# Kernel tuning notes

Hardware: AMD Instinct MI355X
Metric: run time of the kernel (lower is better)

The kernel has to match this reference:

```python
import jax, jax.numpy as jnp
import numpy as np


def setup_inputs() -> dict:
    key = jax.random.key(0)
    k1, k2, k3, k4 = jax.random.split(key, 4)
    B, T, E, H = 8, 2048, 1024, 64
    x = jax.random.normal(k1, (B, T, E), dtype=jnp.float32)
    # scale params like typical init to keep logits sane
    Wk = jax.random.normal(k2, (E, H), dtype=jnp.float32) * (E ** -0.5)
    Wq = jax.random.normal(k3, (E, H), dtype=jnp.float32) * (E ** -0.5)
    Wv = jax.random.normal(k4, (E, H), dtype=jnp.float32) * (E ** -0.5)
    return {"x": x, "Wk": Wk, "Wq": Wq, "Wv": Wv}


def reference(x, Wk, Wq, Wv):
    # x: [B, T, E]; Wk/Wq/Wv: [E, H]
    T = x.shape[1]
    H = Wk.shape[1]
    k = jnp.einsum('bte,eh->bth', x, Wk)
    q = jnp.einsum('bte,eh->bth', x, Wq)
    v = jnp.einsum('bte,eh->bth', x, Wv)
    # scaled scores [B, T, T]
    wei = jnp.einsum('bqh,bkh->bqk', q, k) * (H ** -0.5)
    causal = jnp.tril(jnp.ones((T, T), dtype=bool))  # tril buffer
    wei = jnp.where(causal, wei, -jnp.inf)
    wei = jax.nn.softmax(wei, axis=-1)
    # dropout p=0.0 (eval): identity
    return jnp.einsum('bqk,bkh->bqh', wei, v)
```

## Files before the change

kernel.cpp:

```cpp
#include <hip/hip_runtime.h>
#include <math.h>

constexpr int B_ = 8, T_ = 2048, E_ = 1024, H_ = 64;
constexpr long BT = (long)B_ * T_;

typedef __attribute__((ext_vector_type(8))) short bf16x8;
typedef __attribute__((ext_vector_type(4))) float f32x4;

__device__ inline unsigned short bf16_rne(float f) {
    union { float f; unsigned u; } v; v.f = f;
    unsigned u = v.u + (0x7FFFu + ((v.u >> 16) & 1u));
    return (unsigned short)(u >> 16);
}
__device__ inline unsigned pack_bf16x2(float lo, float hi) {
    return (unsigned)bf16_rne(lo) | ((unsigned)bf16_rne(hi) << 16);
}

__device__ inline void load_lds16(const void* g, void* l) {
    __builtin_amdgcn_global_load_lds(
        (const __attribute__((address_space(1))) void*)(uintptr_t)g,
        (__attribute__((address_space(3))) void*)(unsigned)(uintptr_t)l,
        16, 0, 0);
}

constexpr float QS = 0.18033688011112042f;

__global__ __launch_bounds__(256) void wt_build_k(
    const float* __restrict__ Wk, const float* __restrict__ Wq,
    const float* __restrict__ Wv, unsigned short* __restrict__ Wt)
{
    const int d    = blockIdx.x * 256 + threadIdx.x;
    const int tile = d >> 6;
    const int lq   = d & 63;
    const int quad = lq >> 4;
    const int l16  = lq & 15;
    const int kc   = tile / 12;
    const int nt   = tile - kc * 12;
    const int n    = nt * 16 + l16;

    const float* src; int col; float s = 1.0f;
    if (n < 64)       { src = Wk; col = n; }
    else if (n < 128) { src = Wq; col = n - 64; s = QS; }
    else              { src = Wv; col = n - 128; }

    const int kk0 = kc * 32 + quad * 8;
    const float* sp = src + (size_t)kk0 * H_ + col;
    unsigned p[4];
    #pragma unroll
    for (int jj = 0; jj < 4; jj++)
        p[jj] = pack_bf16x2(sp[(2 * jj) * H_] * s, sp[(2 * jj + 1) * H_] * s);
    *(uint4*)(Wt + (size_t)d * 8) = make_uint4(p[0], p[1], p[2], p[3]);
}

__global__ __launch_bounds__(512, 4) void qkv_mfma_k(
    const float* __restrict__ x, const unsigned short* __restrict__ Wt,
    unsigned short* __restrict__ kO, unsigned short* __restrict__ qO,
    unsigned short* __restrict__ vfO)
{
    __shared__ float4 xs[2][32][16];
    __shared__ unsigned short VL[32][66];

    const int t    = threadIdx.x;
    const int w    = t >> 6;
    const int l    = t & 63;
    const int l16  = l & 15;
    const int quad = l >> 4;
    const int rg   = w >> 2;
    const int nq   = w & 3;
    const int row0 = blockIdx.x * 32 + rg * 16;
    const int row0b = blockIdx.x * 32;

    const int rr = w * 4 + (l >> 4);
    const int cc = l & 15;
    const int gg = cc ^ (rr & 7);
    const float* gsrc = x + (size_t)(row0b + rr) * E_ + gg * 4;

    const int r  = rg * 16 + l16;
    const int rx = r & 7;

    f32x4 acc[3];
    #pragma unroll
    for (int n = 0; n < 3; n++) acc[n] = (f32x4){0.f, 0.f, 0.f, 0.f};

    load_lds16(gsrc, &xs[0][rr][cc]);

    for (int it = 0; it < 16; ++it) {
        const int buf = it & 1;
        __syncthreads();
        if (it + 1 < 16)
            load_lds16(gsrc + (it + 1) * 64, &xs[buf ^ 1][rr][cc]);

        #pragma unroll
        for (int kk = 0; kk < 2; ++kk) {
            const int G0 = kk * 8 + quad * 2;
            float4 fa = xs[buf][r][G0 ^ rx];
            float4 fb = xs[buf][r][(G0 + 1) ^ rx];

            const int kc = it * 2 + kk;
            const unsigned short* wpp = Wt + (size_t)(kc * 12 + nq * 3) * 512 + (size_t)l * 8;
            bf16x8 b0 = *(const bf16x8*)(wpp);
            bf16x8 b1 = *(const bf16x8*)(wpp + 512);
            bf16x8 b2 = *(const bf16x8*)(wpp + 1024);

            union { bf16x8 v; unsigned u[4]; } av;
            av.u[0] = pack_bf16x2(fa.x, fa.y);
            av.u[1] = pack_bf16x2(fa.z, fa.w);
            av.u[2] = pack_bf16x2(fb.x, fb.y);
            av.u[3] = pack_bf16x2(fb.z, fb.w);

            acc[0] = __builtin_amdgcn_mfma_f32_16x16x32_bf16(av.v, b0, acc[0], 0, 0, 0);
            acc[1] = __builtin_amdgcn_mfma_f32_16x16x32_bf16(av.v, b1, acc[1], 0, 0, 0);
            acc[2] = __builtin_amdgcn_mfma_f32_16x16x32_bf16(av.v, b2, acc[2], 0, 0, 0);
        }
    }

    #pragma unroll
    for (int n = 0; n < 3; n++) {
        const int gn = nq * 3 + n;
        const int hb = gn * 16 + l16;
        if (gn < 4) {
            #pragma unroll
            for (int rr2 = 0; rr2 < 4; rr2++) {
                const int row = row0 + quad * 4 + rr2;
                kO[(size_t)row * H_ + hb] = bf16_rne(acc[n][rr2]);
            }
        } else if (gn < 8) {
            #pragma unroll
            for (int rr2 = 0; rr2 < 4; rr2++) {
                const int row = row0 + quad * 4 + rr2;
                qO[(size_t)row * H_ + (hb - 64)] = bf16_rne(acc[n][rr2]);
            }
        } else {
            #pragma unroll
            for (int rr2 = 0; rr2 < 4; rr2++)
                VL[rg * 16 + quad * 4 + rr2][(gn - 8) * 16 + l16] = bf16_rne(acc[n][rr2]);
        }
    }
    __syncthreads();

    if (t < 256) {
        const int g  = t >> 6;
        const int lf = t & 15;
        const int qf = (t >> 4) & 3;
        unsigned pk[4];
        #pragma unroll
        for (int jj = 0; jj < 4; jj++) {
            const int p0 = qf * 8 + 2 * jj;
            const int i0 = (p0 >> 1) | ((p0 & 1) << 4);
            const int p1 = p0 + 1;
            const int i1 = (p1 >> 1) | ((p1 & 1) << 4);
            pk[jj] = (unsigned)VL[i0][g * 16 + lf]
                   | ((unsigned)VL[i1][g * 16 + lf] << 16);
        }
        const int tile = blockIdx.x;
        *(uint4*)(vfO + ((size_t)tile * 4 + g) * 512 + (size_t)(t & 63) * 8) =
            make_uint4(pk[0], pk[1], pk[2], pk[3]);
    }
}

__global__ __launch_bounds__(256, 2) void attn_mfma(
    const unsigned short* __restrict__ q,
    const unsigned short* __restrict__ k,
    const unsigned short* __restrict__ vf,
    float* __restrict__ out)
{
    __shared__ __align__(16) unsigned short KV[4][2][4096];
    __shared__ unsigned short Pl[4][16 * 40];

    const int t    = threadIdx.x;
    const int w    = t >> 6;
    const int l    = t & 63;
    const int l16  = l & 15;
    const int quad = l >> 4;

    const int b    = blockIdx.x & 7;
    const int qidx = blockIdx.x >> 3;
    const int qt   = (qidx & 1) ? (127 - (qidx >> 1)) : (qidx >> 1);
    const int t0   = qt * 16;
    const int nk   = t0 / 32 + 1;

    const size_t qoff = ((size_t)b * T_ + t0 + l16) * H_ + quad * 8;
    bf16x8 aq0 = *(const bf16x8*)(q + qoff);
    bf16x8 aq1 = *(const bf16x8*)(q + qoff + 32);

    f32x4 o[4];
    #pragma unroll
    for (int g = 0; g < 4; g++) o[g] = (f32x4){0.f, 0.f, 0.f, 0.f};
    float ls[4] = {0.f, 0.f, 0.f, 0.f};

    const unsigned short* kbp = k  + (size_t)b * T_ * H_;
    const unsigned short* vfb = vf + (size_t)b * 64 * 2048;
    unsigned short* Pw = &Pl[w][0];
    unsigned short* kv0 = &KV[w][0][0];
    unsigned short* kv1 = &KV[w][1][0];

    auto issue_tile = [&](int kt, unsigned short* dst) {
        const int kbase = kt * 32;
        const unsigned short* kp = kbp + (size_t)(kbase + l16) * H_ + quad * 8;
        load_lds16(kp,               dst + 0 * 512 + l * 8);
        load_lds16(kp + 32,          dst + 1 * 512 + l * 8);
        load_lds16(kp + 16 * H_,     dst + 2 * 512 + l * 8);
        load_lds16(kp + 16 * H_ + 32, dst + 3 * 512 + l * 8);
        const unsigned short* vp = vfb + (size_t)kt * 2048 + l * 8;
        load_lds16(vp,        dst + 4 * 512 + l * 8);
        load_lds16(vp + 512,  dst + 5 * 512 + l * 8);
        load_lds16(vp + 1024, dst + 6 * 512 + l * 8);
        load_lds16(vp + 1536, dst + 7 * 512 + l * 8);
    };

    if (w < nk) issue_tile(w, kv0);

    int it = 0;
    for (int kt = w; kt < nk; kt += 4, ++it) {
        unsigned short* cur = (it & 1) ? kv1 : kv0;
        unsigned short* nxt = (it & 1) ? kv0 : kv1;
        if (kt + 4 < nk) {
            issue_tile(kt + 4, nxt);
            asm volatile("s_waitcnt vmcnt(8)" ::: "memory");
        } else {
            asm volatile("s_waitcnt vmcnt(0)" ::: "memory");
        }

        bf16x8 bk00 = *(const bf16x8*)(cur + 0 * 512 + l * 8);
        bf16x8 bk01 = *(const bf16x8*)(cur + 1 * 512 + l * 8);
        bf16x8 bk10 = *(const bf16x8*)(cur + 2 * 512 + l * 8);
        bf16x8 bk11 = *(const bf16x8*)(cur + 3 * 512 + l * 8);
        bf16x8 bv0  = *(const bf16x8*)(cur + 4 * 512 + l * 8);
        bf16x8 bv1  = *(const bf16x8*)(cur + 5 * 512 + l * 8);
        bf16x8 bv2  = *(const bf16x8*)(cur + 6 * 512 + l * 8);
        bf16x8 bv3  = *(const bf16x8*)(cur + 7 * 512 + l * 8);

        const int kbase = kt * 32;
        f32x4 s0 = (f32x4){0.f, 0.f, 0.f, 0.f};
        f32x4 s1 = (f32x4){0.f, 0.f, 0.f, 0.f};
        s0 = __builtin_amdgcn_mfma_f32_16x16x32_bf16(aq0, bk00, s0, 0, 0, 0);
        s0 = __builtin_amdgcn_mfma_f32_16x16x32_bf16(aq1, bk01, s0, 0, 0, 0);
        s1 = __builtin_amdgcn_mfma_f32_16x16x32_bf16(aq0, bk10, s1, 0, 0, 0);
        s1 = __builtin_amdgcn_mfma_f32_16x16x32_bf16(aq1, bk11, s1, 0, 0, 0);

        if (kbase + 31 > t0) {
            const int rowb = t0 + quad * 4;
            #pragma unroll
            for (int r = 0; r < 4; r++) {
                if (kbase + l16 > rowb + r)      s0[r] = -3.0e38f;
                if (kbase + 16 + l16 > rowb + r) s1[r] = -3.0e38f;
            }
        }

        #pragma unroll
        for (int r = 0; r < 4; r++) {
            float p0 = exp2f(s0[r]);
            float p1 = exp2f(s1[r]);
            ls[r] += p0 + p1;
            *(unsigned*)(Pw + (quad * 4 + r) * 40 + 2 * l16) = pack_bf16x2(p0, p1);
        }
        asm volatile("s_waitcnt lgkmcnt(0)" ::: "memory");
        bf16x8 ap = *(const bf16x8*)(Pw + l16 * 40 + quad * 8);

        o[0] = __builtin_amdgcn_mfma_f32_16x16x32_bf16(ap, bv0, o[0], 0, 0, 0);
        o[1] = __builtin_amdgcn_mfma_f32_16x16x32_bf16(ap, bv1, o[1], 0, 0, 0);
        o[2] = __builtin_amdgcn_mfma_f32_16x16x32_bf16(ap, bv2, o[2], 0, 0, 0);
        o[3] = __builtin_amdgcn_mfma_f32_16x16x32_bf16(ap, bv3, o[3], 0, 0, 0);
    }

    #pragma unroll
    for (int r = 0; r < 4; r++) {
        float s = ls[r];
        s += __shfl_xor(s, 1);
        s += __shfl_xor(s, 2);
        s += __shfl_xor(s, 4);
        s += __shfl_xor(s, 8);
        ls[r] = s;
    }

    __syncthreads();
    float* otb = (float*)&KV[0][0][0];
    float* lsW = otb + 4 * 16 * 68;
    if (l16 == 0) {
        #pragma unroll
        for (int r = 0; r < 4; r++) lsW[w * 16 + quad * 4 + r] = ls[r];
    }
    #pragma unroll
    for (int g = 0; g < 4; g++)
        #pragma unroll
        for (int r = 0; r < 4; r++)
            otb[((w * 16) + quad * 4 + r) * 68 + g * 16 + l16] = o[g][r];
    __syncthreads();

    {
        const int col = w * 16 + l16;
        #pragma unroll
        for (int r = 0; r < 4; r++) {
            const int row = quad * 4 + r;
            float L  = lsW[0 * 16 + row] + lsW[1 * 16 + row]
                     + lsW[2 * 16 + row] + lsW[3 * 16 + row];
            float sv = otb[(0 * 16 + row) * 68 + col] + otb[(1 * 16 + row) * 68 + col]
                     + otb[(2 * 16 + row) * 68 + col] + otb[(3 * 16 + row) * 68 + col];
            out[((size_t)b * T_ + t0 + row) * H_ + col] = sv / L;
        }
    }
}

extern "C" void kernel_launch(void* const* d_in, const int* in_sizes, int n_in,
                              void* d_out, int out_size, void* d_ws, size_t ws_size,
                              hipStream_t stream)
{
    const float* x  = (const float*)d_in[0];
    const float* Wk = (const float*)d_in[1];
    const float* Wq = (const float*)d_in[2];
    const float* Wv = (const float*)d_in[3];

    unsigned short* wt    = (unsigned short*)d_ws;
    unsigned short* kbuf  = wt + 24576 * 8;
    unsigned short* qbuf  = kbuf + BT * H_;
    unsigned short* vfbuf = qbuf + BT * H_;
    float* outp = (float*)d_out;

    wt_build_k<<<96, 256, 0, stream>>>(Wk, Wq, Wv, wt);
    qkv_mfma_k<<<(B_ * T_) / 32, 512, 0, stream>>>(x, wt, kbuf, qbuf, vfbuf);
    attn_mfma<<<B_ * 128, 256, 0, stream>>>(qbuf, kbuf, vfbuf, outp);
}
```

Measured before the change: 147.9 us.

## Load K/V tiles directly into registers with ping-pong prefetch instead of LDS

Replaces the per-wave LDS double buffer filled by global_load_lds with direct global-to-register loads into two register sets that alternate, prefetching the next tile while computing the current one. This drops the LDS round trip and the 64 KB K/V shared buffer, so occupancy is raised to 3 blocks per CU via launch bounds. It also switches bf16 packing to the hardware v_cvt_pk_bf16_f32 instruction. The cost is more vector registers for the two tile sets, which may cause spills under the tighter register limit.

```diff
diff --git a/kernel.cpp b/kernel.cpp
--- a/kernel.cpp
+++ b/kernel.cpp
@@ -13,7 +13,9 @@
     return (unsigned short)(u >> 16);
 }
 __device__ inline unsigned pack_bf16x2(float lo, float hi) {
-    return (unsigned)bf16_rne(lo) | ((unsigned)bf16_rne(hi) << 16);
+    unsigned r;
+    asm("v_cvt_pk_bf16_f32 %0, %1, %2" : "=v"(r) : "v"(lo), "v"(hi));
+    return r;
 }
 
 __device__ inline void load_lds16(const void* g, void* l) {
@@ -158,14 +160,17 @@
     }
 }
 
-__global__ __launch_bounds__(256, 2) void attn_mfma(
+struct KVr { bf16x8 k00, k01, k10, k11, v0, v1, v2, v3; };
+
+__global__ __launch_bounds__(256, 3) void attn_mfma(
     const unsigned short* __restrict__ q,
     const unsigned short* __restrict__ k,
     const unsigned short* __restrict__ vf,
     float* __restrict__ out)
 {
-    __shared__ __align__(16) unsigned short KV[4][2][4096];
     __shared__ unsigned short Pl[4][16 * 40];
+    __shared__ float Ot[4][16][68];
+    __shared__ float LsW[4][16];
 
     const int t    = threadIdx.x;
     const int w    = t >> 6;
@@ -188,56 +193,32 @@
     for (int g = 0; g < 4; g++) o[g] = (f32x4){0.f, 0.f, 0.f, 0.f};
     float ls[4] = {0.f, 0.f, 0.f, 0.f};
 
-    const unsigned short* kbp = k  + (size_t)b * T_ * H_;
-    const unsigned short* vfb = vf + (size_t)b * 64 * 2048;
+    const unsigned short* kbp = k  + (size_t)b * T_ * H_ + (size_t)l16 * H_ + quad * 8;
+    const unsigned short* vfb = vf + (size_t)b * 64 * 2048 + (size_t)l * 8;
     unsigned short* Pw = &Pl[w][0];
-    unsigned short* kv0 = &KV[w][0][0];
-    unsigned short* kv1 = &KV[w][1][0];
-
-    auto issue_tile = [&](int kt, unsigned short* dst) {
-        const int kbase = kt * 32;
-        const unsigned short* kp = kbp + (size_t)(kbase + l16) * H_ + quad * 8;
-        load_lds16(kp,               dst + 0 * 512 + l * 8);
-        load_lds16(kp + 32,          dst + 1 * 512 + l * 8);
-        load_lds16(kp + 16 * H_,     dst + 2 * 512 + l * 8);
-        load_lds16(kp + 16 * H_ + 32, dst + 3 * 512 + l * 8);
-        const unsigned short* vp = vfb + (size_t)kt * 2048 + l * 8;
-        load_lds16(vp,        dst + 4 * 512 + l * 8);
-        load_lds16(vp + 512,  dst + 5 * 512 + l * 8);
-        load_lds16(vp + 1024, dst + 6 * 512 + l * 8);
-        load_lds16(vp + 1536, dst + 7 * 512 + l * 8);
+
+    auto LT = [&](int kt, KVr& R) {
+        const unsigned short* kp = kbp + (size_t)kt * 32 * H_;
+        R.k00 = *(const bf16x8*)(kp);
+        R.k01 = *(const bf16x8*)(kp + 32);
+        R.k10 = *(const bf16x8*)(kp + 16 * H_);
+        R.k11 = *(const bf16x8*)(kp + 16 * H_ + 32);
+        const unsigned short* vp = vfb + (size_t)kt * 2048;
+        R.v0 = *(const bf16x8*)(vp);
+        R.v1 = *(const bf16x8*)(vp + 512);
+        R.v2 = *(const bf16x8*)(vp + 1024);
+        R.v3 = *(const bf16x8*)(vp + 1536);
     };
 
-    if (w < nk) issue_tile(w, kv0);
-
-    int it = 0;
-    for (int kt = w; kt < nk; kt += 4, ++it) {
-        unsigned short* cur = (it & 1) ? kv1 : kv0;
-        unsigned short* nxt = (it & 1) ? kv0 : kv1;
-        if (kt + 4 < nk) {
-            issue_tile(kt + 4, nxt);
-            asm volatile("s_waitcnt vmcnt(8)" ::: "memory");
-        } else {
-            asm volatile("s_waitcnt vmcnt(0)" ::: "memory");
-        }
-
-        bf16x8 bk00 = *(const bf16x8*)(cur + 0 * 512 + l * 8);
-        bf16x8 bk01 = *(const bf16x8*)(cur + 1 * 512 + l * 8);
-        bf16x8 bk10 = *(const bf16x8*)(cur + 2 * 512 + l * 8);
-        bf16x8 bk11 = *(const bf16x8*)(cur + 3 * 512 + l * 8);
-        bf16x8 bv0  = *(const bf16x8*)(cur + 4 * 512 + l * 8);
-        bf16x8 bv1  = *(const bf16x8*)(cur + 5 * 512 + l * 8);
-        bf16x8 bv2  = *(const bf16x8*)(cur + 6 * 512 + l * 8);
-        bf16x8 bv3  = *(const bf16x8*)(cur + 7 * 512 + l * 8);
-
-        const int kbase = kt * 32;
+    auto COMP = [&](int kt, KVr& R) {
         f32x4 s0 = (f32x4){0.f, 0.f, 0.f, 0.f};
         f32x4 s1 = (f32x4){0.f, 0.f, 0.f, 0.f};
-        s0 = __builtin_amdgcn_mfma_f32_16x16x32_bf16(aq0, bk00, s0, 0, 0, 0);
-        s0 = __builtin_amdgcn_mfma_f32_16x16x32_bf16(aq1, bk01, s0, 0, 0, 0);
-        s1 = __builtin_amdgcn_mfma_f32_16x16x32_bf16(aq0, bk10, s1, 0, 0, 0);
-        s1 = __builtin_amdgcn_mfma_f32_16x16x32_bf16(aq1, bk11, s1, 0, 0, 0);
-
+        s0 = __builtin_amdgcn_mfma_f32_16x16x32_bf16(aq0, R.k00, s0, 0, 0, 0);
+        s0 = __builtin_amdgcn_mfma_f32_16x16x32_bf16(aq1, R.k01, s0, 0, 0, 0);
+        s1 = __builtin_amdgcn_mfma_f32_16x16x32_bf16(aq0, R.k10, s1, 0, 0, 0);
+        s1 = __builtin_amdgcn_mfma_f32_16x16x32_bf16(aq1, R.k11, s1, 0, 0, 0);
+
+        const int kbase = kt * 32;
         if (kbase + 31 > t0) {
             const int rowb = t0 + quad * 4;
             #pragma unroll
@@ -257,10 +238,32 @@
         asm volatile("s_waitcnt lgkmcnt(0)" ::: "memory");
         bf16x8 ap = *(const bf16x8*)(Pw + l16 * 40 + quad * 8);
 
-        o[0] = __builtin_amdgcn_mfma_f32_16x16x32_bf16(ap, bv0, o[0], 0, 0, 0);
-        o[1] = __builtin_amdgcn_mfma_f32_16x16x32_bf16(ap, bv1, o[1], 0, 0, 0);
-        o[2] = __builtin_amdgcn_mfma_f32_16x16x32_bf16(ap, bv2, o[2], 0, 0, 0);
-        o[3] = __builtin_amdgcn_mfma_f32_16x16x32_bf16(ap, bv3, o[3], 0, 0, 0);
+        o[0] = __builtin_amdgcn_mfma_f32_16x16x32_bf16(ap, R.v0, o[0], 0, 0, 0);
+        o[1] = __builtin_amdgcn_mfma_f32_16x16x32_bf16(ap, R.v1, o[1], 0, 0, 0);
+        o[2] = __builtin_amdgcn_mfma_f32_16x16x32_bf16(ap, R.v2, o[2], 0, 0, 0);
+        o[3] = __builtin_amdgcn_mfma_f32_16x16x32_bf16(ap, R.v3, o[3], 0, 0, 0);
+    };
+
+    KVr A, B;
+    int kt = w;
+    if (kt < nk) {
+        LT(kt, A);
+        while (true) {
+            if (kt + 4 < nk) {
+                LT(kt + 4, B);
+                __builtin_amdgcn_sched_barrier(0);
+            }
+            COMP(kt, A);
+            kt += 4;
+            if (kt >= nk) break;
+            if (kt + 4 < nk) {
+                LT(kt + 4, A);
+                __builtin_amdgcn_sched_barrier(0);
+            }
+            COMP(kt, B);
+            kt += 4;
+            if (kt >= nk) break;
+        }
     }
 
     #pragma unroll
@@ -273,18 +276,15 @@
         ls[r] = s;
     }
 
-    __syncthreads();
-    float* otb = (float*)&KV[0][0][0];
-    float* lsW = otb + 4 * 16 * 68;
     if (l16 == 0) {
         #pragma unroll
-        for (int r = 0; r < 4; r++) lsW[w * 16 + quad * 4 + r] = ls[r];
+        for (int r = 0; r < 4; r++) LsW[w][quad * 4 + r] = ls[r];
     }
     #pragma unroll
     for (int g = 0; g < 4; g++)
         #pragma unroll
         for (int r = 0; r < 4; r++)
-            otb[((w * 16) + quad * 4 + r) * 68 + g * 16 + l16] = o[g][r];
+            Ot[w][quad * 4 + r][g * 16 + l16] = o[g][r];
     __syncthreads();
 
     {
@@ -292,10 +292,9 @@
         #pragma unroll
         for (int r = 0; r < 4; r++) {
             const int row = quad * 4 + r;
-            float L  = lsW[0 * 16 + row] + lsW[1 * 16 + row]
-                     + lsW[2 * 16 + row] + lsW[3 * 16 + row];
-            float sv = otb[(0 * 16 + row) * 68 + col] + otb[(1 * 16 + row) * 68 + col]
-                     + otb[(2 * 16 + row) * 68 + col] + otb[(3 * 16 + row) * 68 + col];
+            float L  = LsW[0][row] + LsW[1][row] + LsW[2][row] + LsW[3][row];
+            float sv = Ot[0][row][col] + Ot[1][row][col]
+                     + Ot[2][row][col] + Ot[3][row][col];
             out[((size_t)b * T_ + t0 + row) * H_ + col] = sv / L;
         }
     }
```

After: 149.3 us. About the same (+0.9%).
